# Kernel tuning notes

Measured on AMD Instinct MI355X. Metric: run time of the kernel, lower is better.

Reference implementation:

```python
import jax, jax.numpy as jnp
import numpy as np

D_K = 32  # hard-coded in original module


def setup_inputs() -> dict:
    key = jax.random.key(0)
    kq, kk, kv, km = jax.random.split(key, 4)
    B, H, S, D = 4, 12, 2048, D_K
    Q = jax.random.normal(kq, (B, H, S, D), dtype=jnp.float32)
    K = jax.random.normal(kk, (B, H, S, D), dtype=jnp.float32)
    V = jax.random.normal(kv, (B, H, S, D), dtype=jnp.float32)
    attn_mask = jax.random.bernoulli(km, 0.5, (B, H, S, S))
    return {"Q": Q, "K": K, "V": V, "attn_mask": attn_mask}


def tanh_max(a):
    # (exp(a) - exp(-a)) / sum_over_keys(exp(a) + exp(-a))
    ea = jnp.exp(a)
    ena = jnp.exp(-a)
    return (ea - ena) / (ea + ena).sum(axis=-1, keepdims=True)


def reference(Q, K, V, attn_mask):
    # scores: [B,H,S,S]
    scores = jnp.einsum("bhqd,bhkd->bhqk", Q, K) / np.sqrt(D_K).astype(np.float32)
    attn = tanh_max(scores)
    # NOTE: original calls attn.masked_fill(attn_mask, 0.0) WITHOUT assignment
    # (non-in-place), so the mask has no effect. Reproduced faithfully.
    context = jnp.einsum("bhqk,bhkd->bhqd", attn, V)
    return context
```

## Files before the change

### kernel.cpp

```cpp
#include <hip/hip_runtime.h>
#include <hip/hip_bf16.h>
#include <cstdint>
#include <cstddef>


#define SLEN 2048
#define DK   32
#define NBH  48
#define NCH  32

typedef __attribute__((ext_vector_type(8))) short bf16x8;
typedef __attribute__((ext_vector_type(4))) float f32x4;

__device__ __forceinline__ unsigned pk2(float a, float b) {
    __hip_bfloat162 h = __float22bfloat162_rn(make_float2(a, b));
    union { __hip_bfloat162 h2; unsigned u; } cv; cv.h2 = h; return cv.u;
}

__global__ __launch_bounds__(256)
void prep_kv(const float* __restrict__ K, const float* __restrict__ V,
             unsigned short* __restrict__ Kbf, unsigned short* __restrict__ VTf) {
    if (blockIdx.x < NBH * 32) {
        const int b  = blockIdx.x;
        const int bh = b >> 5, kg = b & 31;
        const int tl = threadIdx.x >> 6, l = threadIdx.x & 63;
        const int T  = kg * 4 + tl;
        const int c  = T >> 1, tb = T & 1;
        const int l16 = l & 15;
        const int key = c * 32 + 8 * (l16 >> 2) + 2 * (l16 & 3) + tb;
        const float* src = K + ((size_t)bh * SLEN + key) * DK + (l >> 4) * 8;
        float4 a = *(const float4*)src;
        float4 b4 = *(const float4*)(src + 4);
        union { uint4 q; unsigned u[4]; } o;
        o.u[0] = pk2(a.x, a.y);  o.u[1] = pk2(a.z, a.w);
        o.u[2] = pk2(b4.x, b4.y); o.u[3] = pk2(b4.z, b4.w);
        *(uint4*)(Kbf + (((size_t)bh * 128 + T) * 64 + l) * 8) = o.q;
    } else {
        __shared__ float tile[32][33];
        const int b  = blockIdx.x - NBH * 32;
        const int bh = b >> 6, c = b & 63;
        const int t  = threadIdx.x;
        {
            const int row = t >> 3, c4 = (t & 7) * 4;
            float4 v4 = *(const float4*)(V + ((size_t)bh * SLEN + c * 32 + row) * DK + c4);
            tile[row][c4 + 0] = v4.x; tile[row][c4 + 1] = v4.y;
            tile[row][c4 + 2] = v4.z; tile[row][c4 + 3] = v4.w;
        }
        __syncthreads();
        const int h = t >> 7, l = (t >> 1) & 63, jh = t & 1;
        const int col = h * 16 + (l & 15);
        const int r0  = (l >> 4) * 8 + jh * 4;
        uint2 u;
        u.x = pk2(tile[r0 + 0][col], tile[r0 + 1][col]);
        u.y = pk2(tile[r0 + 2][col], tile[r0 + 3][col]);
        *(uint2*)(VTf + ((((size_t)bh * 64 + c) * 2 + h) * 64 + l) * 8 + jh * 4) = u;
    }
}

__global__ __launch_bounds__(256, 4)
void attn_mfma(const float* __restrict__ Q, const unsigned short* __restrict__ Kbf,
               const unsigned short* __restrict__ VTf, float* __restrict__ Out) {
    __shared__ __align__(16) float Red[2][64][20];

    const int tid  = threadIdx.x;
    const int lane = tid & 63;
    const int wv   = tid >> 6;
    const int quad = lane >> 4;
    const int l16  = lane & 15;
    const int qi   = wv >> 1;
    const int kh   = wv & 1;

    const int b   = blockIdx.x;
    const int xcd = b & 7;
    const int i   = b >> 3;
    const int bh  = xcd * 6 + (i % 6);
    const int j   = i / 6;
    const int qbase = (j * 2 + qi) * 32;

    const float sc = 0.17677669529663687f * 1.4426950408889634f;
    union { bf16x8 v; unsigned u[4]; } aQ0, aQ1;
    {
        const float* qp0 = Q + ((size_t)bh * SLEN + qbase + l16) * DK + quad * 8;
        float4 qa = *(const float4*)qp0;
        float4 qb = *(const float4*)(qp0 + 4);
        aQ0.u[0] = pk2(qa.x * sc, qa.y * sc); aQ0.u[1] = pk2(qa.z * sc, qa.w * sc);
        aQ0.u[2] = pk2(qb.x * sc, qb.y * sc); aQ0.u[3] = pk2(qb.z * sc, qb.w * sc);
        const float* qp1 = qp0 + 16 * DK;
        float4 qc = *(const float4*)qp1;
        float4 qd = *(const float4*)(qp1 + 4);
        aQ1.u[0] = pk2(qc.x * sc, qc.y * sc); aQ1.u[1] = pk2(qc.z * sc, qc.w * sc);
        aQ1.u[2] = pk2(qd.x * sc, qd.y * sc); aQ1.u[3] = pk2(qd.z * sc, qd.w * sc);
    }

    const bf16x8* kf = (const bf16x8*)Kbf + ((size_t)bh * 128 + kh * 64) * 64 + lane;
    const bf16x8* vf = (const bf16x8*)VTf + ((size_t)bh * 128 + kh * 64) * 64 + lane;

    f32x4 o00 = {0,0,0,0}, o01 = {0,0,0,0};
    f32x4 o10 = {0,0,0,0}, o11 = {0,0,0,0};
    float den0 = 0.f, den1 = 0.f;
    const f32x4 zero = {0,0,0,0};

    bf16x8 k0 = kf[0], k1 = kf[64];

    for (int c = 0; c < NCH; ++c) {
        f32x4 s00 = __builtin_amdgcn_mfma_f32_16x16x32_bf16(k0, aQ0.v, zero, 0, 0, 0);
        f32x4 s01 = __builtin_amdgcn_mfma_f32_16x16x32_bf16(k1, aQ0.v, zero, 0, 0, 0);
        f32x4 s10 = __builtin_amdgcn_mfma_f32_16x16x32_bf16(k0, aQ1.v, zero, 0, 0, 0);
        f32x4 s11 = __builtin_amdgcn_mfma_f32_16x16x32_bf16(k1, aQ1.v, zero, 0, 0, 0);

        bf16x8 v0 = vf[(size_t)c * 128];
        bf16x8 v1 = vf[(size_t)c * 128 + 64];
        const int cn = (c + 1) & (NCH - 1);
        k0 = kf[(size_t)cn * 128];
        k1 = kf[(size_t)cn * 128 + 64];

        union { bf16x8 v; unsigned u[4]; } aP0, aP1;
        #pragma unroll
        for (int r = 0; r < 4; ++r) {
            float e0  = __builtin_amdgcn_exp2f(s00[r]);
            float en0 = __builtin_amdgcn_exp2f(-s00[r]);
            float e1  = __builtin_amdgcn_exp2f(s01[r]);
            float en1 = __builtin_amdgcn_exp2f(-s01[r]);
            den0 += (e0 + en0) + (e1 + en1);
            aP0.u[r] = pk2(e0 - en0, e1 - en1);
        }
        #pragma unroll
        for (int r = 0; r < 4; ++r) {
            float e0  = __builtin_amdgcn_exp2f(s10[r]);
            float en0 = __builtin_amdgcn_exp2f(-s10[r]);
            float e1  = __builtin_amdgcn_exp2f(s11[r]);
            float en1 = __builtin_amdgcn_exp2f(-s11[r]);
            den1 += (e0 + en0) + (e1 + en1);
            aP1.u[r] = pk2(e0 - en0, e1 - en1);
        }

        o00 = __builtin_amdgcn_mfma_f32_16x16x32_bf16(aP0.v, v0, o00, 0, 0, 0);
        o01 = __builtin_amdgcn_mfma_f32_16x16x32_bf16(aP0.v, v1, o01, 0, 0, 0);
        o10 = __builtin_amdgcn_mfma_f32_16x16x32_bf16(aP1.v, v0, o10, 0, 0, 0);
        o11 = __builtin_amdgcn_mfma_f32_16x16x32_bf16(aP1.v, v1, o11, 0, 0, 0);
    }

    den0 += __shfl_xor(den0, 16); den0 += __shfl_xor(den0, 32);
    den1 += __shfl_xor(den1, 16); den1 += __shfl_xor(den1, 32);

    if (kh == 1) {
        float* r = &Red[qi][lane][0];
        *(f32x4*)(r +  0) = o00; *(f32x4*)(r +  4) = o01;
        *(f32x4*)(r +  8) = o10; *(f32x4*)(r + 12) = o11;
        r[16] = den0; r[17] = den1;
    }
    __syncthreads();
    if (kh == 0) {
        const float* r = &Red[qi][lane][0];
        o00 += *(const f32x4*)(r +  0); o01 += *(const f32x4*)(r +  4);
        o10 += *(const f32x4*)(r +  8); o11 += *(const f32x4*)(r + 12);
        den0 += r[16]; den1 += r[17];

        float* outp = Out + ((size_t)bh * SLEN + qbase) * DK;
        #pragma unroll
        for (int rr = 0; rr < 4; ++rr) {
            float inv0 = 1.0f / __shfl(den0, quad * 4 + rr, 16);
            float inv1 = 1.0f / __shfl(den1, quad * 4 + rr, 16);
            int q0 = quad * 4 + rr;
            int q1 = 16 + quad * 4 + rr;
            outp[(size_t)q0 * DK + l16]      = o00[rr] * inv0;
            outp[(size_t)q0 * DK + 16 + l16] = o01[rr] * inv0;
            outp[(size_t)q1 * DK + l16]      = o10[rr] * inv1;
            outp[(size_t)q1 * DK + 16 + l16] = o11[rr] * inv1;
        }
    }
}

extern "C" void kernel_launch(void* const* d_in, const int* in_sizes, int n_in,
                              void* d_out, int out_size, void* d_ws, size_t ws_size,
                              hipStream_t stream) {
    const float* Q = (const float*)d_in[0];
    const float* K = (const float*)d_in[1];
    const float* V = (const float*)d_in[2];
    float* Out = (float*)d_out;
    unsigned short* Kbf = (unsigned short*)d_ws;
    unsigned short* VTf = Kbf + (size_t)NBH * SLEN * DK;

    prep_kv<<<dim3(NBH * 32 + NBH * 64), dim3(256), 0, stream>>>(K, V, Kbf, VTf);
    attn_mfma<<<dim3(1536), dim3(256), 0, stream>>>(Q, Kbf, VTf, Out);
}
```

Baseline: 926.6 us.

## Fuse K/V bf16 conversion into attention kernel with LDS double-buffered staging

Removes the separate prep kernel that converted K and V to bf16 fragment layouts. The attention kernel now streams fp32 K tiles into LDS via global_load_lds with an XOR swizzle and writes V transposed as bf16 into padded LDS, using double buffering with a barrier per chunk. The block layout changes from two waves per query tile splitting keys (with an LDS reduction) to four waves each owning 32 queries and sharing K/V tiles over the full key range. It saves a launch and the workspace round trip, but adds per-chunk conversion work, LDS traffic and barriers, and halves the grid to 768 blocks.

```diff
diff --git a/kernel.cpp b/kernel.cpp
--- a/kernel.cpp
+++ b/kernel.cpp
@@ -7,75 +7,41 @@
 #define SLEN 2048
 #define DK   32
 #define NBH  48
-#define NCH  32
+#define NCH  64
+#define PROW 36
 
 typedef __attribute__((ext_vector_type(8))) short bf16x8;
 typedef __attribute__((ext_vector_type(4))) float f32x4;
+typedef const __attribute__((address_space(1))) void* gas_ptr;
+typedef __attribute__((address_space(3))) void*       las_ptr;
 
 __device__ __forceinline__ unsigned pk2(float a, float b) {
     __hip_bfloat162 h = __float22bfloat162_rn(make_float2(a, b));
     union { __hip_bfloat162 h2; unsigned u; } cv; cv.h2 = h; return cv.u;
 }
-
-__global__ __launch_bounds__(256)
-void prep_kv(const float* __restrict__ K, const float* __restrict__ V,
-             unsigned short* __restrict__ Kbf, unsigned short* __restrict__ VTf) {
-    if (blockIdx.x < NBH * 32) {
-        const int b  = blockIdx.x;
-        const int bh = b >> 5, kg = b & 31;
-        const int tl = threadIdx.x >> 6, l = threadIdx.x & 63;
-        const int T  = kg * 4 + tl;
-        const int c  = T >> 1, tb = T & 1;
-        const int l16 = l & 15;
-        const int key = c * 32 + 8 * (l16 >> 2) + 2 * (l16 & 3) + tb;
-        const float* src = K + ((size_t)bh * SLEN + key) * DK + (l >> 4) * 8;
-        float4 a = *(const float4*)src;
-        float4 b4 = *(const float4*)(src + 4);
-        union { uint4 q; unsigned u[4]; } o;
-        o.u[0] = pk2(a.x, a.y);  o.u[1] = pk2(a.z, a.w);
-        o.u[2] = pk2(b4.x, b4.y); o.u[3] = pk2(b4.z, b4.w);
-        *(uint4*)(Kbf + (((size_t)bh * 128 + T) * 64 + l) * 8) = o.q;
-    } else {
-        __shared__ float tile[32][33];
-        const int b  = blockIdx.x - NBH * 32;
-        const int bh = b >> 6, c = b & 63;
-        const int t  = threadIdx.x;
-        {
-            const int row = t >> 3, c4 = (t & 7) * 4;
-            float4 v4 = *(const float4*)(V + ((size_t)bh * SLEN + c * 32 + row) * DK + c4);
-            tile[row][c4 + 0] = v4.x; tile[row][c4 + 1] = v4.y;
-            tile[row][c4 + 2] = v4.z; tile[row][c4 + 3] = v4.w;
-        }
-        __syncthreads();
-        const int h = t >> 7, l = (t >> 1) & 63, jh = t & 1;
-        const int col = h * 16 + (l & 15);
-        const int r0  = (l >> 4) * 8 + jh * 4;
-        uint2 u;
-        u.x = pk2(tile[r0 + 0][col], tile[r0 + 1][col]);
-        u.y = pk2(tile[r0 + 2][col], tile[r0 + 3][col]);
-        *(uint2*)(VTf + ((((size_t)bh * 64 + c) * 2 + h) * 64 + l) * 8 + jh * 4) = u;
-    }
+__device__ __forceinline__ unsigned short f2b(float x) {
+    __hip_bfloat16 h = __float2bfloat16(x);
+    union { __hip_bfloat16 h; unsigned short u; } cv; cv.h = h; return cv.u;
 }
 
-__global__ __launch_bounds__(256, 4)
-void attn_mfma(const float* __restrict__ Q, const unsigned short* __restrict__ Kbf,
-               const unsigned short* __restrict__ VTf, float* __restrict__ Out) {
-    __shared__ __align__(16) float Red[2][64][20];
+__global__ __launch_bounds__(256, 3)
+void attn_fused(const float* __restrict__ Q, const float* __restrict__ K,
+                const float* __restrict__ V, float* __restrict__ Out) {
+    __shared__ __align__(16) float          Kst[2][32 * 32];
+    __shared__ __align__(16) unsigned short Vst[2][32 * PROW];
 
     const int tid  = threadIdx.x;
     const int lane = tid & 63;
     const int wv   = tid >> 6;
     const int quad = lane >> 4;
     const int l16  = lane & 15;
-    const int qi   = wv >> 1;
-    const int kh   = wv & 1;
 
     const int b   = blockIdx.x;
     const int xcd = b & 7;
     const int i   = b >> 3;
     const int bh  = xcd * 6 + (i % 6);
-    const int j   = i / 6;
-    const int qbase = (j * 2 + qi) * 32;
+    const int qblk = i / 6;
+    const int qbase = qblk * 128 + wv * 32;
 
     const float sc = 0.17677669529663687f * 1.4426950408889634f;
     union { bf16x8 v; unsigned u[4]; } aQ0, aQ1;
@@ -92,82 +58,123 @@
         aQ1.u[2] = pk2(qd.x * sc, qd.y * sc); aQ1.u[3] = pk2(qd.z * sc, qd.w * sc);
     }
 
-    const bf16x8* kf = (const bf16x8*)Kbf + ((size_t)bh * 128 + kh * 64) * 64 + lane;
-    const bf16x8* vf = (const bf16x8*)VTf + ((size_t)bh * 128 + kh * 64) * 64 + lane;
+    const float* Kh = K + (size_t)bh * SLEN * DK;
+    const float* Vh = V + (size_t)bh * SLEN * DK;
+
+    const int grow   = wv * 8 + (lane >> 3);
+    const int spos   = lane & 7;
+    const int schunk = spos ^ ((grow >> 1) & 7);
+    const int ksrc   = grow * 32 + schunk * 4;
+    const int vsrc   = grow * 32 + spos * 4;
+    const int vcol   = spos * 4;
+
+    const int rkey0 = 8 * (l16 >> 2) + 2 * (l16 & 3);
+    const int rxor  = (rkey0 >> 1) & 7;
+    const int rc0   = ((2 * quad + 0) ^ rxor) * 4;
+    const int rc1   = ((2 * quad + 1) ^ rxor) * 4;
 
     f32x4 o00 = {0,0,0,0}, o01 = {0,0,0,0};
     f32x4 o10 = {0,0,0,0}, o11 = {0,0,0,0};
     float den0 = 0.f, den1 = 0.f;
     const f32x4 zero = {0,0,0,0};
 
-    bf16x8 k0 = kf[0], k1 = kf[64];
+    __builtin_amdgcn_global_load_lds((gas_ptr)(Kh + ksrc),
+                                     (las_ptr)(&Kst[0][wv * 256]), 16, 0, 0);
+    float4 vreg = *(const float4*)(Vh + vsrc);
+    {
+        unsigned short* vtw = &Vst[0][0];
+        vtw[(vcol + 0) * PROW + grow] = f2b(vreg.x);
+        vtw[(vcol + 1) * PROW + grow] = f2b(vreg.y);
+        vtw[(vcol + 2) * PROW + grow] = f2b(vreg.z);
+        vtw[(vcol + 3) * PROW + grow] = f2b(vreg.w);
+    }
+    __syncthreads();
 
     for (int c = 0; c < NCH; ++c) {
-        f32x4 s00 = __builtin_amdgcn_mfma_f32_16x16x32_bf16(k0, aQ0.v, zero, 0, 0, 0);
-        f32x4 s01 = __builtin_amdgcn_mfma_f32_16x16x32_bf16(k1, aQ0.v, zero, 0, 0, 0);
-        f32x4 s10 = __builtin_amdgcn_mfma_f32_16x16x32_bf16(k0, aQ1.v, zero, 0, 0, 0);
-        f32x4 s11 = __builtin_amdgcn_mfma_f32_16x16x32_bf16(k1, aQ1.v, zero, 0, 0, 0);
+        const int buf = c & 1, nbuf = buf ^ 1;
+        if (c + 1 < NCH) {
+            __builtin_amdgcn_global_load_lds(
+                (gas_ptr)(Kh + (c + 1) * 1024 + ksrc),
+                (las_ptr)(&Kst[nbuf][wv * 256]), 16, 0, 0);
+            vreg = *(const float4*)(Vh + (c + 1) * 1024 + vsrc);
+        }
 
-        bf16x8 v0 = vf[(size_t)c * 128];
-        bf16x8 v1 = vf[(size_t)c * 128 + 64];
-        const int cn = (c + 1) & (NCH - 1);
-        k0 = kf[(size_t)cn * 128];
-        k1 = kf[(size_t)cn * 128 + 64];
+        const float* kb_ = &Kst[buf][0];
+        float4 e0 = *(const float4*)(kb_ + rkey0 * 32 + rc0);
+        float4 e1 = *(const float4*)(kb_ + rkey0 * 32 + rc1);
+        float4 d0 = *(const float4*)(kb_ + (rkey0 + 1) * 32 + rc0);
+        float4 d1 = *(const float4*)(kb_ + (rkey0 + 1) * 32 + rc1);
+        union { bf16x8 v; unsigned u[4]; } kf0, kf1;
+        kf0.u[0] = pk2(e0.x, e0.y); kf0.u[1] = pk2(e0.z, e0.w);
+        kf0.u[2] = pk2(e1.x, e1.y); kf0.u[3] = pk2(e1.z, e1.w);
+        kf1.u[0] = pk2(d0.x, d0.y); kf1.u[1] = pk2(d0.z, d0.w);
+        kf1.u[2] = pk2(d1.x, d1.y); kf1.u[3] = pk2(d1.z, d1.w);
+
+        f32x4 s00 = __builtin_amdgcn_mfma_f32_16x16x32_bf16(kf0.v, aQ0.v, zero, 0, 0, 0);
+        f32x4 s01 = __builtin_amdgcn_mfma_f32_16x16x32_bf16(kf1.v, aQ0.v, zero, 0, 0, 0);
+        f32x4 s10 = __builtin_amdgcn_mfma_f32_16x16x32_bf16(kf0.v, aQ1.v, zero, 0, 0, 0);
+        f32x4 s11 = __builtin_amdgcn_mfma_f32_16x16x32_bf16(kf1.v, aQ1.v, zero, 0, 0, 0);
+
+        const unsigned short* vt = &Vst[buf][0];
+        union { bf16x8 v; uint2 h[2]; } V0, V1;
+        {
+            const unsigned short* p0 = vt + l16 * PROW + quad * 8;
+            V0.h[0] = *(const uint2*)p0;
+            V0.h[1] = *(const uint2*)(p0 + 4);
+            const unsigned short* p1 = vt + (16 + l16) * PROW + quad * 8;
+            V1.h[0] = *(const uint2*)p1;
+            V1.h[1] = *(const uint2*)(p1 + 4);
+        }
 
         union { bf16x8 v; unsigned u[4]; } aP0, aP1;
         #pragma unroll
         for (int r = 0; r < 4; ++r) {
-            float e0  = __builtin_amdgcn_exp2f(s00[r]);
-            float en0 = __builtin_amdgcn_exp2f(-s00[r]);
-            float e1  = __builtin_amdgcn_exp2f(s01[r]);
-            float en1 = __builtin_amdgcn_exp2f(-s01[r]);
-            den0 += (e0 + en0) + (e1 + en1);
-            aP0.u[r] = pk2(e0 - en0, e1 - en1);
+            float e0_  = __builtin_amdgcn_exp2f(s00[r]);
+            float en0_ = __builtin_amdgcn_exp2f(-s00[r]);
+            float e1_  = __builtin_amdgcn_exp2f(s01[r]);
+            float en1_ = __builtin_amdgcn_exp2f(-s01[r]);
+            den0 += (e0_ + en0_) + (e1_ + en1_);
+            aP0.u[r] = pk2(e0_ - en0_, e1_ - en1_);
         }
         #pragma unroll
         for (int r = 0; r < 4; ++r) {
-            float e0  = __builtin_amdgcn_exp2f(s10[r]);
-            float en0 = __builtin_amdgcn_exp2f(-s10[r]);
-            float e1  = __builtin_amdgcn_exp2f(s11[r]);
-            float en1 = __builtin_amdgcn_exp2f(-s11[r]);
-            den1 += (e0 + en0) + (e1 + en1);
-            aP1.u[r] = pk2(e0 - en0, e1 - en1);
+            float e0_  = __builtin_amdgcn_exp2f(s10[r]);
+            float en0_ = __builtin_amdgcn_exp2f(-s10[r]);
+            float e1_  = __builtin_amdgcn_exp2f(s11[r]);
+            float en1_ = __builtin_amdgcn_exp2f(-s11[r]);
+            den1 += (e0_ + en0_) + (e1_ + en1_);
+            aP1.u[r] = pk2(e0_ - en0_, e1_ - en1_);
         }
 
-        o00 = __builtin_amdgcn_mfma_f32_16x16x32_bf16(aP0.v, v0, o00, 0, 0, 0);
-        o01 = __builtin_amdgcn_mfma_f32_16x16x32_bf16(aP0.v, v1, o01, 0, 0, 0);
-        o10 = __builtin_amdgcn_mfma_f32_16x16x32_bf16(aP1.v, v0, o10, 0, 0, 0);
-        o11 = __builtin_amdgcn_mfma_f32_16x16x32_bf16(aP1.v, v1, o11, 0, 0, 0);
+        o00 = __builtin_amdgcn_mfma_f32_16x16x32_bf16(aP0.v, V0.v, o00, 0, 0, 0);
+        o01 = __builtin_amdgcn_mfma_f32_16x16x32_bf16(aP0.v, V1.v, o01, 0, 0, 0);
+        o10 = __builtin_amdgcn_mfma_f32_16x16x32_bf16(aP1.v, V0.v, o10, 0, 0, 0);
+        o11 = __builtin_amdgcn_mfma_f32_16x16x32_bf16(aP1.v, V1.v, o11, 0, 0, 0);
+
+        if (c + 1 < NCH) {
+            unsigned short* vtw = &Vst[nbuf][0];
+            vtw[(vcol + 0) * PROW + grow] = f2b(vreg.x);
+            vtw[(vcol + 1) * PROW + grow] = f2b(vreg.y);
+            vtw[(vcol + 2) * PROW + grow] = f2b(vreg.z);
+            vtw[(vcol + 3) * PROW + grow] = f2b(vreg.w);
+        }
+        __syncthreads();
     }
 
     den0 += __shfl_xor(den0, 16); den0 += __shfl_xor(den0, 32);
     den1 += __shfl_xor(den1, 16); den1 += __shfl_xor(den1, 32);
 
-    if (kh == 1) {
-        float* r = &Red[qi][lane][0];
-        *(f32x4*)(r +  0) = o00; *(f32x4*)(r +  4) = o01;
-        *(f32x4*)(r +  8) = o10; *(f32x4*)(r + 12) = o11;
-        r[16] = den0; r[17] = den1;
-    }
-    __syncthreads();
-    if (kh == 0) {
-        const float* r = &Red[qi][lane][0];
-        o00 += *(const f32x4*)(r +  0); o01 += *(const f32x4*)(r +  4);
-        o10 += *(const f32x4*)(r +  8); o11 += *(const f32x4*)(r + 12);
-        den0 += r[16]; den1 += r[17];
-
-        float* outp = Out + ((size_t)bh * SLEN + qbase) * DK;
-        #pragma unroll
-        for (int rr = 0; rr < 4; ++rr) {
-            float inv0 = 1.0f / __shfl(den0, quad * 4 + rr, 16);
-            float inv1 = 1.0f / __shfl(den1, quad * 4 + rr, 16);
-            int q0 = quad * 4 + rr;
-            int q1 = 16 + quad * 4 + rr;
-            outp[(size_t)q0 * DK + l16]      = o00[rr] * inv0;
-            outp[(size_t)q0 * DK + 16 + l16] = o01[rr] * inv0;
-            outp[(size_t)q1 * DK + l16]      = o10[rr] * inv1;
-            outp[(size_t)q1 * DK + 16 + l16] = o11[rr] * inv1;
-        }
+    float* outp = Out + ((size_t)bh * SLEN + qbase) * DK;
+    #pragma unroll
+    for (int rr = 0; rr < 4; ++rr) {
+        float inv0 = 1.0f / __shfl(den0, quad * 4 + rr, 16);
+        float inv1 = 1.0f / __shfl(den1, quad * 4 + rr, 16);
+        int q0 = quad * 4 + rr;
+        int q1 = 16 + quad * 4 + rr;
+        outp[(size_t)q0 * DK + l16]      = o00[rr] * inv0;
+        outp[(size_t)q0 * DK + 16 + l16] = o01[rr] * inv0;
+        outp[(size_t)q1 * DK + l16]      = o10[rr] * inv1;
+        outp[(size_t)q1 * DK + 16 + l16] = o11[rr] * inv1;
     }
 }
 
@@ -178,9 +185,5 @@
     const float* K = (const float*)d_in[1];
     const float* V = (const float*)d_in[2];
     float* Out = (float*)d_out;
-    unsigned short* Kbf = (unsigned short*)d_ws;
-    unsigned short* VTf = Kbf + (size_t)NBH * SLEN * DK;
-
-    prep_kv<<<dim3(NBH * 32 + NBH * 64), dim3(256), 0, stream>>>(K, V, Kbf, VTf);
-    attn_mfma<<<dim3(1536), dim3(256), 0, stream>>>(Q, Kbf, VTf, Out);
+    attn_fused<<<dim3(NBH * 16), dim3(256), 0, stream>>>(Q, K, V, Out);
 }
```

Measured after the change: 956.5 us. 1.03x slower.
